# Optimization experiments

Measured on AMD Instinct MI355X. Metric: run time of the kernel, lower is better.

Reference implementation:

```python
import jax, jax.numpy as jnp
import numpy as np

N = 8192      # nodes
IN = 1433     # input_feat_dim
H1 = 256      # hidden_dim1
H2 = 128      # hidden_dim2
EPS = 1e-5    # BatchNorm1d eps
NEG = -9e15   # GAT mask value
SLOPE = 0.2   # leaky_relu negative slope (gamma)


def setup_inputs() -> dict:
    key = jax.random.key(0)
    ks = jax.random.split(key, 8)
    x = jax.random.normal(ks[0], (N, H2), dtype=jnp.float32)
    u = jax.random.uniform(ks[1], (N, N), dtype=jnp.float32)
    adj = jnp.where(u > 0.999, jnp.float32(0.01), jnp.float32(0.0))
    def w(k, shape):
        fan = shape[0]
        return jax.random.normal(k, shape, dtype=jnp.float32) / jnp.sqrt(jnp.float32(fan))
    return {
        "x": x,
        "adj": adj,
        "W_att": w(ks[2], (H2, H2)),
        "a_att": w(ks[3], (2 * H2, 1)),
        "W_fd1": w(ks[4], (H2, H1)),
        "bn1_g": jnp.ones((H1,), jnp.float32),
        "bn1_b": jnp.zeros((H1,), jnp.float32),
        "W_fd2": w(ks[5], (H1, IN)),
        "bn2_g": jnp.ones((IN,), jnp.float32),
        "bn2_b": jnp.zeros((IN,), jnp.float32),
        "W_sd1": w(ks[6], (H2, H1)),
        "bn3_g": jnp.ones((H1,), jnp.float32),
        "bn3_b": jnp.zeros((H1,), jnp.float32),
    }


def batchnorm(h, g, b):
    # BatchNorm1d training-mode forward: batch stats, biased variance
    m = h.mean(axis=0)
    v = ((h - m) ** 2).mean(axis=0)
    return (h - m) * jax.lax.rsqrt(v + EPS) * g + b


def reference(x, adj, W_att, a_att, W_fd1, bn1_g, bn1_b, W_fd2, bn2_g, bn2_b,
              W_sd1, bn3_g, bn3_b):
    # --- GraphAttentionLayer (concat=False, dropout=0) ---
    Wh = x @ W_att                       # [N, H2]
    f1 = Wh @ a_att[:H2]                 # [N, 1]
    f2 = Wh @ a_att[H2:]                 # [N, 1]
    e = jax.nn.leaky_relu(f1 + f2.T, SLOPE)          # [N, N]
    att = jnp.where(adj > 0, e, jnp.float32(NEG))
    att = jax.nn.softmax(att, axis=1)
    z = att @ Wh                         # condensed encoder output [N, H2]
    # --- feature decoder branch ---
    h1 = jax.nn.relu(adj @ (z @ W_fd1))  # GCN: adj @ (X W), relu
    h1 = batchnorm(h1, bn1_g, bn1_b)
    feat = jax.nn.relu(adj @ (h1 @ W_fd2))
    feat = batchnorm(feat, bn2_g, bn2_b)
    # --- structure decoder branch ---
    s1 = jax.nn.relu(adj @ (z @ W_sd1))
    s1 = batchnorm(s1, bn3_g, bn3_b)
    struct = s1 @ s1.T                   # inner-product decode, identity act [N, N]
    return feat, struct
```

## Files before the change

kernel.cpp:

```cpp
#include <hip/hip_runtime.h>
#include <hip/hip_bf16.h>
#include <stdint.h>

#define NN 8192
#define MAXNZ 64
#define BN_EPS 1e-5f
#define SLOPE 0.2f
#define IND 1433
#define NPAD 1536

typedef float f32x4v __attribute__((ext_vector_type(4)));
typedef short bf16x8v __attribute__((ext_vector_type(8)));

__device__ __forceinline__ float wave_sum(float v) {
#pragma unroll
  for (int off = 32; off > 0; off >>= 1) v += __shfl_xor(v, off);
  return v;
}
__device__ __forceinline__ float wave_max(float v) {
#pragma unroll
  for (int off = 32; off > 0; off >>= 1) v = fmaxf(v, __shfl_xor(v, off));
  return v;
}

#define GLOAD_LDS16(g, l)                                                      \
  __builtin_amdgcn_global_load_lds(                                            \
      (const __attribute__((address_space(1))) unsigned int*)(g),              \
      (__attribute__((address_space(3))) unsigned int*)(l), 16, 0, 0)

__global__ __launch_bounds__(256) void gemm64_f32(const float* __restrict__ A,
                                                  const float* __restrict__ B,
                                                  float* __restrict__ C, int M,
                                                  int N, int K) {
  __shared__ float As[64][68];
  __shared__ float Bs[64][68];
  const int t = threadIdx.x;
  const int m0 = blockIdx.x * 64, n0 = blockIdx.y * 64;
  const int tx = t & 15, ty = t >> 4;
  float acc[4][4] = {};
  for (int kt = 0; kt < K; kt += 64) {
    if (kt) __syncthreads();
#pragma unroll
    for (int i = 0; i < 4; ++i) {
      int fid = t + 256 * i;
      int r = fid >> 4, kq = (fid & 15) * 4;
      float4 v = *(const float4*)&A[(size_t)(m0 + r) * K + kt + kq];
      *(float4*)&As[r][kq] = v;
    }
#pragma unroll
    for (int i = 0; i < 4; ++i) {
      int fid = t + 256 * i;
      int r = fid >> 4, cq = (fid & 15) * 4;
      float4 v = *(const float4*)&B[(size_t)(kt + r) * N + n0 + cq];
      *(float4*)&Bs[r][cq] = v;
    }
    __syncthreads();
#pragma unroll 4
    for (int k0 = 0; k0 < 64; k0 += 4) {
      float4 a[4], b[4];
#pragma unroll
      for (int i = 0; i < 4; ++i) a[i] = *(const float4*)&As[ty * 4 + i][k0];
#pragma unroll
      for (int j = 0; j < 4; ++j) b[j] = *(const float4*)&Bs[k0 + j][tx * 4];
#pragma unroll
      for (int kk = 0; kk < 4; ++kk) {
#pragma unroll
        for (int i = 0; i < 4; ++i) {
          float av = ((const float*)&a[i])[kk];
#pragma unroll
          for (int j = 0; j < 4; ++j)
            acc[i][j] += av * ((const float*)&b[kk])[j];
        }
      }
    }
  }
#pragma unroll
  for (int i = 0; i < 4; ++i) {
    float4 v = make_float4(acc[i][0], acc[i][1], acc[i][2], acc[i][3]);
    *(float4*)&C[(size_t)(m0 + ty * 4 + i) * N + n0 + tx * 4] = v;
  }
}

__global__ void colsum_k(const float* __restrict__ Wh, float* __restrict__ cs) {
  int t = threadIdx.x, b = blockIdx.x;
  int c = t & 127, rg = t >> 7;
  float s = 0.f;
  int r0 = b * 128;
  for (int r = rg; r < 128; r += 2) s += Wh[(size_t)(r0 + r) * 128 + c];
  atomicAdd(&cs[c], s);
}

__global__ void f1f2_k(const float* __restrict__ Wh, const float* __restrict__ a_att,
                       float* __restrict__ f1, float* __restrict__ f2) {
  int l = threadIdx.x & 63, w = threadIdx.x >> 6;
  int i = blockIdx.x * 4 + w;
  float w0 = Wh[(size_t)i * 128 + l], w1 = Wh[(size_t)i * 128 + 64 + l];
  float p1 = w0 * a_att[l] + w1 * a_att[64 + l];
  float p2 = w0 * a_att[128 + l] + w1 * a_att[192 + l];
  p1 = wave_sum(p1);
  p2 = wave_sum(p2);
  if (l == 0) { f1[i] = p1; f2[i] = p2; }
}

__global__ void extract_attn_k(const float* __restrict__ adj, const float* __restrict__ Wh,
                               const float* __restrict__ f1, const float* __restrict__ f2,
                               const float* __restrict__ cs, int* __restrict__ nnzA,
                               int* __restrict__ idxA, float* __restrict__ valA,
                               float* __restrict__ valsumA, float* __restrict__ z) {
  __shared__ int idxL[4][MAXNZ];
  __shared__ float valL[4][MAXNZ];
  int l = threadIdx.x & 63, w = threadIdx.x >> 6;
  int i = blockIdx.x * 4 + w;
  const float* row = adj + (size_t)i * NN;
  int base = 0;
  for (int it = 0; it < NN / 256; ++it) {
    float4 v4 = *(const float4*)&row[it * 256 + l * 4];
#pragma unroll
    for (int j = 0; j < 4; ++j) {
      float v = ((const float*)&v4)[j];
      bool p = v > 0.0f;
      unsigned long long m = __ballot(p);
      if (p) {
        int pos = base + (int)__popcll(m & ((1ull << l) - 1ull));
        if (pos < MAXNZ) {
          idxL[w][pos] = it * 256 + l * 4 + j;
          valL[w][pos] = v;
        }
      }
      base += (int)__popcll(m);
    }
  }
  int nnz = base < MAXNZ ? base : MAXNZ;
  if (l == 0) nnzA[i] = nnz;
  __syncthreads();

  int c = -1;
  float v = 0.f, att = 0.f;
  if (l < nnz) { c = idxL[w][l]; v = valL[w][l]; }
  idxA[(size_t)i * MAXNZ + l] = (l < nnz) ? c : 0;
  valA[(size_t)i * MAXNZ + l] = v;
  float vs = wave_sum(v);
  if (l == 0) valsumA[i] = vs;

  if (nnz == 0) {
    const float inv = 1.0f / 8192.0f;
    z[(size_t)i * 128 + l] = cs[l] * inv;
    z[(size_t)i * 128 + 64 + l] = cs[64 + l] * inv;
    return;
  }
  float e = -INFINITY;
  if (l < nnz) {
    float u = f1[i] + f2[c];
    e = u >= 0.f ? u : SLOPE * u;
  }
  float mx = wave_max(e);
  float p = (l < nnz) ? expf(e - mx) : 0.f;
  float s = wave_sum(p);
  att = p / s;
  float a0 = 0.f, a1 = 0.f;
  for (int j = 0; j < nnz; ++j) {
    float wt = __shfl(att, j);
    int r = __shfl(c, j);
    a0 += wt * Wh[(size_t)r * 128 + l];
    a1 += wt * Wh[(size_t)r * 128 + 64 + l];
  }
  z[(size_t)i * 128 + l] = a0;
  z[(size_t)i * 128 + 64 + l] = a1;
}

__global__ void gather_z_k(const float* __restrict__ X, const int* __restrict__ nnzA,
                           const int* __restrict__ idxA, const float* __restrict__ valA,
                           __hip_bfloat16* __restrict__ Y) {
  int l = threadIdx.x & 63, w = threadIdx.x >> 6;
  int i = blockIdx.x * 4 + w;
  int nnz = nnzA[i];
  float a0 = 0.f, a1 = 0.f;
  for (int j = 0; j < nnz; ++j) {
    int r = idxA[(size_t)i * MAXNZ + j];
    float v = valA[(size_t)i * MAXNZ + j];
    a0 += v * X[(size_t)r * 128 + l];
    a1 += v * X[(size_t)r * 128 + 64 + l];
  }
  Y[(size_t)i * 128 + l] = __float2bfloat16(a0);
  Y[(size_t)i * 128 + 64 + l] = __float2bfloat16(a1);
}

__global__ void gather_h_k(const float* __restrict__ t, const int* __restrict__ nnzA,
                           const int* __restrict__ idxA, const float* __restrict__ valA,
                           const float* __restrict__ valsumA, const float* __restrict__ sums,
                           const float* __restrict__ sumsq, const float* __restrict__ g,
                           const float* __restrict__ b, __hip_bfloat16* __restrict__ Y) {
  __shared__ int idxL[MAXNZ];
  __shared__ float valL[MAXNZ];
  int i = blockIdx.x, tt = threadIdx.x;
  int nnz = nnzA[i];
  if (tt < MAXNZ) {
    idxL[tt] = idxA[(size_t)i * MAXNZ + tt];
    valL[tt] = valA[(size_t)i * MAXNZ + tt];
  }
  __syncthreads();
  float acc = 0.f;
  for (int j = 0; j < nnz; ++j)
    acc += valL[j] * fmaxf(t[(size_t)idxL[j] * 512 + tt], 0.f);
  float m = sums[tt] * (1.f / 8192.f);
  float va = fmaxf(sumsq[tt] * (1.f / 8192.f) - m * m, 0.f);
  float sc = g[tt] * rsqrtf(va + BN_EPS);
  float sh = b[tt] - m * sc;
  Y[(size_t)i * 256 + tt] = __float2bfloat16(acc * sc + sh * valsumA[i]);
}

__global__ void s1_apply_k(const float* __restrict__ t, const float* __restrict__ sums,
                           const float* __restrict__ sumsq, const float* __restrict__ g,
                           const float* __restrict__ b, __hip_bfloat16* __restrict__ s1b) {
  int i = blockIdx.x, c = threadIdx.x;
  float m = sums[256 + c] * (1.f / 8192.f);
  float va = fmaxf(sumsq[256 + c] * (1.f / 8192.f) - m * m, 0.f);
  float sc = g[c] * rsqrtf(va + BN_EPS);
  float sh = b[c] - m * sc;
  float v = fmaxf(t[(size_t)i * 512 + 256 + c], 0.f) * sc + sh;
  s1b[(size_t)i * 256 + c] = __float2bfloat16(v);
}

__global__ void feat_apply_k(const __hip_bfloat16* __restrict__ fp, const float* __restrict__ sums,
                             const float* __restrict__ sumsq, const float* __restrict__ g,
                             const float* __restrict__ b, float* __restrict__ out) {
  int i = blockIdx.x;
  for (int c = threadIdx.x; c < IND; c += 256) {
    float m = sums[c] * (1.f / 8192.f);
    float va = fmaxf(sumsq[c] * (1.f / 8192.f) - m * m, 0.f);
    float sc = g[c] * rsqrtf(va + BN_EPS);
    float sh = b[c] - m * sc;
    out[(size_t)i * IND + c] = __bfloat162float(fp[(size_t)i * NPAD + c]) * sc + sh;
  }
}

__global__ void prep_k(const float* __restrict__ W_fd2, const float* __restrict__ W_fd1,
                       const float* __restrict__ W_sd1, __hip_bfloat16* __restrict__ Wt,
                       __hip_bfloat16* __restrict__ Wcatb) {
  int b = blockIdx.x, t = threadIdx.x;
  int o = b * 256 + t;
  int n = o >> 8, k = o & 255;
  Wt[o] = __float2bfloat16(n < IND ? W_fd2[(size_t)k * IND + n] : 0.f);
  if (b < 256) {
    int nn = o >> 7, kk = o & 127;
    float v = nn < 256 ? W_fd1[(size_t)kk * 256 + nn] : W_sd1[(size_t)kk * 256 + (nn - 256)];
    Wcatb[o] = __float2bfloat16(v);
  }
}

template <int KT, int MODE>
__global__ __launch_bounds__(256) void mfma_bt_k(const short* __restrict__ A,
                                                 const short* __restrict__ Bt,
                                                 void* __restrict__ Cv, int ldc,
                                                 int gridN, float* __restrict__ sums,
                                                 float* __restrict__ sumsq) {
  __shared__ short lds[2][16384];
  const int nwg = gridDim.x;
  const int cpx = nwg >> 3;
  const int bid = blockIdx.x;
  const int wg = (bid & 7) * cpx + (bid >> 3);
  const int m0 = (wg / gridN) * 128, n0 = (wg % gridN) * 128;
  const int t = threadIdx.x;
  const int l = t & 63, w = t >> 6;
  const int wm = w >> 1, wn = w & 1;
  const int KW = KT * 128;
  f32x4v acc[4][4];
#pragma unroll
  for (int i = 0; i < 4; ++i)
#pragma unroll
    for (int j = 0; j < 4; ++j)
#pragma unroll
      for (int q = 0; q < 4; ++q) acc[i][j][q] = 0.f;

  for (int kt = 0; kt < KT; ++kt) {
    if (kt) __syncthreads();
#pragma unroll
    for (int i = 0; i < 8; ++i) {
      int region = w * 8 + i;
      int lr = region * 4 + (l >> 4);
      int ch = (l & 15) ^ (lr & 7);
      const short* gA = A + ((size_t)(m0 + lr) * KW + kt * 128 + ch * 8);
      GLOAD_LDS16(gA, &lds[0][region * 512]);
      const short* gB = Bt + ((size_t)(n0 + lr) * KW + kt * 128 + ch * 8);
      GLOAD_LDS16(gB, &lds[1][region * 512]);
    }
    __syncthreads();
#pragma unroll
    for (int ks = 0; ks < 4; ++ks) {
      bf16x8v af[4], bf[4];
#pragma unroll
      for (int mi = 0; mi < 4; ++mi) {
        int lr = wm * 64 + mi * 16 + (l & 15);
        int ch = (ks * 4 + (l >> 4)) ^ (lr & 7);
        af[mi] = *(const bf16x8v*)&lds[0][lr * 128 + ch * 8];
      }
#pragma unroll
      for (int nj = 0; nj < 4; ++nj) {
        int lr = wn * 64 + nj * 16 + (l & 15);
        int ch = (ks * 4 + (l >> 4)) ^ (lr & 7);
        bf[nj] = *(const bf16x8v*)&lds[1][lr * 128 + ch * 8];
      }
#pragma unroll
      for (int mi = 0; mi < 4; ++mi)
#pragma unroll
        for (int nj = 0; nj < 4; ++nj)
          acc[mi][nj] = __builtin_amdgcn_mfma_f32_16x16x32_bf16(
              af[mi], bf[nj], acc[mi][nj], 0, 0, 0);
    }
  }
#pragma unroll
  for (int nj = 0; nj < 4; ++nj) {
    int col = n0 + wn * 64 + nj * 16 + (l & 15);
    float s = 0.f, ss = 0.f;
#pragma unroll
    for (int mi = 0; mi < 4; ++mi) {
#pragma unroll
      for (int q = 0; q < 4; ++q) {
        int row = m0 + wm * 64 + mi * 16 + (l >> 4) * 4 + q;
        float raw = acc[mi][nj][q];
        float v = fmaxf(raw, 0.f);
        if (MODE == 1) {
          ((__hip_bfloat16*)Cv)[(size_t)row * ldc + col] = __float2bfloat16(v);
        } else {
          ((float*)Cv)[(size_t)row * ldc + col] = raw;
        }
        s += v;
        ss += v * v;
      }
    }
    s += __shfl_xor(s, 16);
    s += __shfl_xor(s, 32);
    ss += __shfl_xor(ss, 16);
    ss += __shfl_xor(ss, 32);
    if ((l >> 4) == 0) {
      atomicAdd(&sums[col], s);
      atomicAdd(&sumsq[col], ss);
    }
  }
}

__global__ __launch_bounds__(256) void mfma_sym_k(const short* __restrict__ A,
                                                  float* __restrict__ C) {
  __shared__ union {
    short stag[2][16384];
    float tr[64 * 129];
  } sh;
  const int bid = blockIdx.x;
  const int wg = (bid & 7) * 260 + (bid >> 3);
  int bi = (int)((129.0f - sqrtf(16641.0f - 8.0f * (float)wg)) * 0.5f);
  while ((bi + 1) * 64 - ((bi + 1) * bi) / 2 <= wg) ++bi;
  while (bi * 64 - (bi * (bi - 1)) / 2 > wg) --bi;
  const int bj = bi + (wg - (bi * 64 - (bi * (bi - 1)) / 2));
  const int m0 = bi * 128, n0 = bj * 128;
  const int t = threadIdx.x;
  const int l = t & 63, w = t >> 6;
  const int wm = w >> 1, wn = w & 1;
  f32x4v acc[4][4];
#pragma unroll
  for (int i = 0; i < 4; ++i)
#pragma unroll
    for (int j = 0; j < 4; ++j)
#pragma unroll
      for (int q = 0; q < 4; ++q) acc[i][j][q] = 0.f;

  for (int kt = 0; kt < 2; ++kt) {
    if (kt) __syncthreads();
#pragma unroll
    for (int i = 0; i < 8; ++i) {
      int region = w * 8 + i;
      int lr = region * 4 + (l >> 4);
      int ch = (l & 15) ^ (lr & 7);
      const short* gA = A + ((size_t)(m0 + lr) * 256 + kt * 128 + ch * 8);
      GLOAD_LDS16(gA, &sh.stag[0][region * 512]);
      const short* gB = A + ((size_t)(n0 + lr) * 256 + kt * 128 + ch * 8);
      GLOAD_LDS16(gB, &sh.stag[1][region * 512]);
    }
    __syncthreads();
#pragma unroll
    for (int ks = 0; ks < 4; ++ks) {
      bf16x8v af[4], bf[4];
#pragma unroll
      for (int mi = 0; mi < 4; ++mi) {
        int lr = wm * 64 + mi * 16 + (l & 15);
        int ch = (ks * 4 + (l >> 4)) ^ (lr & 7);
        af[mi] = *(const bf16x8v*)&sh.stag[0][lr * 128 + ch * 8];
      }
#pragma unroll
      for (int nj = 0; nj < 4; ++nj) {
        int lr = wn * 64 + nj * 16 + (l & 15);
        int ch = (ks * 4 + (l >> 4)) ^ (lr & 7);
        bf[nj] = *(const bf16x8v*)&sh.stag[1][lr * 128 + ch * 8];
      }
#pragma unroll
      for (int mi = 0; mi < 4; ++mi)
#pragma unroll
        for (int nj = 0; nj < 4; ++nj)
          acc[mi][nj] = __builtin_amdgcn_mfma_f32_16x16x32_bf16(
              af[mi], bf[nj], acc[mi][nj], 0, 0, 0);
    }
  }
#pragma unroll
  for (int mi = 0; mi < 4; ++mi) {
#pragma unroll
    for (int nj = 0; nj < 4; ++nj) {
      int col = n0 + wn * 64 + nj * 16 + (l & 15);
#pragma unroll
      for (int q = 0; q < 4; ++q) {
        int row = m0 + wm * 64 + mi * 16 + (l >> 4) * 4 + q;
        C[(size_t)row * NN + col] = acc[mi][nj][q];
      }
    }
  }
  if (bi != bj) {
    for (int half = 0; half < 2; ++half) {
      __syncthreads();
      if (wn == half) {
#pragma unroll
        for (int nj = 0; nj < 4; ++nj) {
          int cc = nj * 16 + (l & 15);
#pragma unroll
          for (int mi = 0; mi < 4; ++mi) {
#pragma unroll
            for (int q = 0; q < 4; ++q) {
              int rr = wm * 64 + mi * 16 + (l >> 4) * 4 + q;
              sh.tr[cc * 129 + rr] = acc[mi][nj][q];
            }
          }
        }
      }
      __syncthreads();
      for (int it = t; it < 64 * 32; it += 256) {
        int cc = it >> 5, rr = (it & 31) * 4;
        float4 v;
        v.x = sh.tr[cc * 129 + rr];
        v.y = sh.tr[cc * 129 + rr + 1];
        v.z = sh.tr[cc * 129 + rr + 2];
        v.w = sh.tr[cc * 129 + rr + 3];
        *(float4*)&C[(size_t)(n0 + half * 64 + cc) * NN + m0 + rr] = v;
      }
    }
  }
}

extern "C" void kernel_launch(void* const* d_in, const int* in_sizes, int n_in,
                              void* d_out, int out_size, void* d_ws, size_t ws_size,
                              hipStream_t stream) {
  const float* x = (const float*)d_in[0];
  const float* adj = (const float*)d_in[1];
  const float* W_att = (const float*)d_in[2];
  const float* a_att = (const float*)d_in[3];
  const float* W_fd1 = (const float*)d_in[4];
  const float* bn1g = (const float*)d_in[5];
  const float* bn1b = (const float*)d_in[6];
  const float* W_fd2 = (const float*)d_in[7];
  const float* bn2g = (const float*)d_in[8];
  const float* bn2b = (const float*)d_in[9];
  const float* W_sd1 = (const float*)d_in[10];
  const float* bn3g = (const float*)d_in[11];
  const float* bn3b = (const float*)d_in[12];

  float* out = (float*)d_out;
  float* feat_out = out;
  float* struct_out = out + (size_t)NN * IND;

  float* ws = (float*)d_ws;
  size_t off = 0;
  auto alloc = [&](size_t nfloats) {
    float* p = ws + off;
    off += (nfloats + 255) & ~(size_t)255;
    return p;
  };
  float* Wh = alloc((size_t)NN * 128);
  float* z = alloc((size_t)NN * 128);
  float* tbuf = alloc((size_t)NN * 512);
  float* f1 = alloc(NN);
  float* f2 = alloc(NN);
  float* valsum = alloc(NN);
  float* zbase = alloc(256 + 512 + 512 + 1536 + 1536);
  float* cs = zbase;
  float* sumsA = zbase + 256;
  float* sumsqA = zbase + 768;
  float* sumsB = zbase + 1280;
  float* sumsqB = zbase + 2816;
  float* valA = alloc((size_t)NN * MAXNZ);
  int* idxA = (int*)alloc((size_t)NN * MAXNZ);
  int* nnzA = (int*)alloc(NN);
  __hip_bfloat16* gb = (__hip_bfloat16*)alloc((size_t)NN * 64);
  __hip_bfloat16* s1b = (__hip_bfloat16*)alloc((size_t)NN * 128);
  __hip_bfloat16* ghb = (__hip_bfloat16*)alloc((size_t)NN * 128);
  __hip_bfloat16* Wt = (__hip_bfloat16*)alloc((size_t)NPAD * 128);
  __hip_bfloat16* Wcatb = (__hip_bfloat16*)alloc(512 * 64);
  __hip_bfloat16* featb = (__hip_bfloat16*)alloc((size_t)NN * NPAD / 2);

  hipMemsetAsync(zbase, 0, (256 + 512 + 512 + 1536 + 1536) * sizeof(float), stream);

  prep_k<<<NPAD, 256, 0, stream>>>(W_fd2, W_fd1, W_sd1, Wt, Wcatb);

  gemm64_f32<<<dim3(NN / 64, 2), 256, 0, stream>>>(x, W_att, Wh, NN, 128, 128);
  colsum_k<<<64, 256, 0, stream>>>(Wh, cs);
  f1f2_k<<<NN / 4, 256, 0, stream>>>(Wh, a_att, f1, f2);
  extract_attn_k<<<NN / 4, 256, 0, stream>>>(adj, Wh, f1, f2, cs, nnzA, idxA, valA,
                                             valsum, z);
  gather_z_k<<<NN / 4, 256, 0, stream>>>(z, nnzA, idxA, valA, gb);

  mfma_bt_k<1, 2><<<64 * 4, 256, 0, stream>>>((const short*)gb, (const short*)Wcatb,
                                              tbuf, 512, 4, sumsA, sumsqA);
  s1_apply_k<<<NN, 256, 0, stream>>>(tbuf, sumsA, sumsqA, bn3g, bn3b, s1b);
  gather_h_k<<<NN, 256, 0, stream>>>(tbuf, nnzA, idxA, valA, valsum, sumsA, sumsqA,
                                     bn1g, bn1b, ghb);

  mfma_bt_k<2, 1><<<64 * 12, 256, 0, stream>>>((const short*)ghb, (const short*)Wt,
                                               featb, NPAD, 12, sumsB, sumsqB);
  feat_apply_k<<<NN, 256, 0, stream>>>(featb, sumsB, sumsqB, bn2g, bn2b, feat_out);

  mfma_sym_k<<<2080, 256, 0, stream>>>((const short*)s1b, struct_out);
}
```

Baseline: 276.5 us.

## Fuse colsum/f1f2, merge s1 apply into gather, bf16 intermediate, direct sym stores

```diff
diff --git a/kernel.cpp b/kernel.cpp
--- a/kernel.cpp
+++ b/kernel.cpp
@@ -81,25 +81,29 @@
   }
 }
 
-__global__ void colsum_k(const float* __restrict__ Wh, float* __restrict__ cs) {
-  int t = threadIdx.x, b = blockIdx.x;
-  int c = t & 127, rg = t >> 7;
-  float s = 0.f;
-  int r0 = b * 128;
-  for (int r = rg; r < 128; r += 2) s += Wh[(size_t)(r0 + r) * 128 + c];
-  atomicAdd(&cs[c], s);
-}
-
-__global__ void f1f2_k(const float* __restrict__ Wh, const float* __restrict__ a_att,
-                       float* __restrict__ f1, float* __restrict__ f2) {
-  int l = threadIdx.x & 63, w = threadIdx.x >> 6;
-  int i = blockIdx.x * 4 + w;
-  float w0 = Wh[(size_t)i * 128 + l], w1 = Wh[(size_t)i * 128 + 64 + l];
-  float p1 = w0 * a_att[l] + w1 * a_att[64 + l];
-  float p2 = w0 * a_att[128 + l] + w1 * a_att[192 + l];
-  p1 = wave_sum(p1);
-  p2 = wave_sum(p2);
-  if (l == 0) { f1[i] = p1; f2[i] = p2; }
+__global__ void colf_k(const float* __restrict__ Wh, const float* __restrict__ a_att,
+                       float* __restrict__ cs, float* __restrict__ f1,
+                       float* __restrict__ f2) {
+  __shared__ float csL[128];
+  int t = threadIdx.x, l = t & 63, w = t >> 6;
+  if (t < 128) csL[t] = 0.f;
+  __syncthreads();
+  float a0 = a_att[l], a1 = a_att[64 + l], a2 = a_att[128 + l], a3 = a_att[192 + l];
+  float s0 = 0.f, s1 = 0.f;
+#pragma unroll
+  for (int rr = 0; rr < 4; ++rr) {
+    int i = blockIdx.x * 16 + w * 4 + rr;
+    float w0 = Wh[(size_t)i * 128 + l], w1 = Wh[(size_t)i * 128 + 64 + l];
+    s0 += w0;
+    s1 += w1;
+    float p1 = wave_sum(w0 * a0 + w1 * a1);
+    float p2 = wave_sum(w0 * a2 + w1 * a3);
+    if (l == 0) { f1[i] = p1; f2[i] = p2; }
+  }
+  atomicAdd(&csL[l], s0);
+  atomicAdd(&csL[64 + l], s1);
+  __syncthreads();
+  if (t < 128) atomicAdd(&cs[t], csL[t]);
 }
 
 __global__ void extract_attn_k(const float* __restrict__ adj, const float* __restrict__ Wh,
@@ -185,11 +189,13 @@
   Y[(size_t)i * 128 + 64 + l] = __float2bfloat16(a1);
 }
 
-__global__ void gather_h_k(const float* __restrict__ t, const int* __restrict__ nnzA,
-                           const int* __restrict__ idxA, const float* __restrict__ valA,
-                           const float* __restrict__ valsumA, const float* __restrict__ sums,
-                           const float* __restrict__ sumsq, const float* __restrict__ g,
-                           const float* __restrict__ b, __hip_bfloat16* __restrict__ Y) {
+__global__ void s1_gather_k(const __hip_bfloat16* __restrict__ t, const int* __restrict__ nnzA,
+                            const int* __restrict__ idxA, const float* __restrict__ valA,
+                            const float* __restrict__ valsumA, const float* __restrict__ sums,
+                            const float* __restrict__ sumsq, const float* __restrict__ g1,
+                            const float* __restrict__ b1, const float* __restrict__ g3,
+                            const float* __restrict__ b3, __hip_bfloat16* __restrict__ s1b,
+                            __hip_bfloat16* __restrict__ ghb) {
   __shared__ int idxL[MAXNZ];
   __shared__ float valL[MAXNZ];
   int i = blockIdx.x, tt = threadIdx.x;
@@ -199,26 +205,22 @@
     valL[tt] = valA[(size_t)i * MAXNZ + tt];
   }
   __syncthreads();
+  {
+    float m = sums[256 + tt] * (1.f / 8192.f);
+    float va = fmaxf(sumsq[256 + tt] * (1.f / 8192.f) - m * m, 0.f);
+    float sc = g3[tt] * rsqrtf(va + BN_EPS);
+    float sh = b3[tt] - m * sc;
+    float v = __bfloat162float(t[(size_t)i * 512 + 256 + tt]) * sc + sh;
+    s1b[(size_t)i * 256 + tt] = __float2bfloat16(v);
+  }
   float acc = 0.f;
   for (int j = 0; j < nnz; ++j)
-    acc += valL[j] * fmaxf(t[(size_t)idxL[j] * 512 + tt], 0.f);
+    acc += valL[j] * __bfloat162float(t[(size_t)idxL[j] * 512 + tt]);
   float m = sums[tt] * (1.f / 8192.f);
   float va = fmaxf(sumsq[tt] * (1.f / 8192.f) - m * m, 0.f);
-  float sc = g[tt] * rsqrtf(va + BN_EPS);
-  float sh = b[tt] - m * sc;
-  Y[(size_t)i * 256 + tt] = __float2bfloat16(acc * sc + sh * valsumA[i]);
-}
-
-__global__ void s1_apply_k(const float* __restrict__ t, const float* __restrict__ sums,
-                           const float* __restrict__ sumsq, const float* __restrict__ g,
-                           const float* __restrict__ b, __hip_bfloat16* __restrict__ s1b) {
-  int i = blockIdx.x, c = threadIdx.x;
-  float m = sums[256 + c] * (1.f / 8192.f);
-  float va = fmaxf(sumsq[256 + c] * (1.f / 8192.f) - m * m, 0.f);
-  float sc = g[c] * rsqrtf(va + BN_EPS);
-  float sh = b[c] - m * sc;
-  float v = fmaxf(t[(size_t)i * 512 + 256 + c], 0.f) * sc + sh;
-  s1b[(size_t)i * 256 + c] = __float2bfloat16(v);
+  float sc = g1[tt] * rsqrtf(va + BN_EPS);
+  float sh = b1[tt] - m * sc;
+  ghb[(size_t)i * 256 + tt] = __float2bfloat16(acc * sc + sh * valsumA[i]);
 }
 
 __global__ void feat_apply_k(const __hip_bfloat16* __restrict__ fp, const float* __restrict__ sums,
@@ -248,10 +250,10 @@
   }
 }
 
-template <int KT, int MODE>
+template <int KT>
 __global__ __launch_bounds__(256) void mfma_bt_k(const short* __restrict__ A,
                                                  const short* __restrict__ Bt,
-                                                 void* __restrict__ Cv, int ldc,
+                                                 __hip_bfloat16* __restrict__ C, int ldc,
                                                  int gridN, float* __restrict__ sums,
                                                  float* __restrict__ sumsq) {
   __shared__ short lds[2][16384];
@@ -317,13 +319,8 @@
 #pragma unroll
       for (int q = 0; q < 4; ++q) {
         int row = m0 + wm * 64 + mi * 16 + (l >> 4) * 4 + q;
-        float raw = acc[mi][nj][q];
-        float v = fmaxf(raw, 0.f);
-        if (MODE == 1) {
-          ((__hip_bfloat16*)Cv)[(size_t)row * ldc + col] = __float2bfloat16(v);
-        } else {
-          ((float*)Cv)[(size_t)row * ldc + col] = raw;
-        }
+        float v = fmaxf(acc[mi][nj][q], 0.f);
+        C[(size_t)row * ldc + col] = __float2bfloat16(v);
         s += v;
         ss += v * v;
       }
@@ -341,10 +338,7 @@
 
 __global__ __launch_bounds__(256) void mfma_sym_k(const short* __restrict__ A,
                                                   float* __restrict__ C) {
-  __shared__ union {
-    short stag[2][16384];
-    float tr[64 * 129];
-  } sh;
+  __shared__ short stag[2][16384];
   const int bid = blockIdx.x;
   const int wg = (bid & 7) * 260 + (bid >> 3);
   int bi = (int)((129.0f - sqrtf(16641.0f - 8.0f * (float)wg)) * 0.5f);
@@ -371,9 +365,9 @@
       int lr = region * 4 + (l >> 4);
       int ch = (l & 15) ^ (lr & 7);
       const short* gA = A + ((size_t)(m0 + lr) * 256 + kt * 128 + ch * 8);
-      GLOAD_LDS16(gA, &sh.stag[0][region * 512]);
+      GLOAD_LDS16(gA, &stag[0][region * 512]);
       const short* gB = A + ((size_t)(n0 + lr) * 256 + kt * 128 + ch * 8);
-      GLOAD_LDS16(gB, &sh.stag[1][region * 512]);
+      GLOAD_LDS16(gB, &stag[1][region * 512]);
     }
     __syncthreads();
 #pragma unroll
@@ -383,13 +377,13 @@
       for (int mi = 0; mi < 4; ++mi) {
         int lr = wm * 64 + mi * 16 + (l & 15);
         int ch = (ks * 4 + (l >> 4)) ^ (lr & 7);
-        af[mi] = *(const bf16x8v*)&sh.stag[0][lr * 128 + ch * 8];
+        af[mi] = *(const bf16x8v*)&stag[0][lr * 128 + ch * 8];
       }
 #pragma unroll
       for (int nj = 0; nj < 4; ++nj) {
         int lr = wn * 64 + nj * 16 + (l & 15);
         int ch = (ks * 4 + (l >> 4)) ^ (lr & 7);
-        bf[nj] = *(const bf16x8v*)&sh.stag[1][lr * 128 + ch * 8];
+        bf[nj] = *(const bf16x8v*)&stag[1][lr * 128 + ch * 8];
       }
 #pragma unroll
       for (int mi = 0; mi < 4; ++mi)
@@ -412,31 +406,15 @@
     }
   }
   if (bi != bj) {
-    for (int half = 0; half < 2; ++half) {
-      __syncthreads();
-      if (wn == half) {
-#pragma unroll
-        for (int nj = 0; nj < 4; ++nj) {
-          int cc = nj * 16 + (l & 15);
-#pragma unroll
-          for (int mi = 0; mi < 4; ++mi) {
-#pragma unroll
-            for (int q = 0; q < 4; ++q) {
-              int rr = wm * 64 + mi * 16 + (l >> 4) * 4 + q;
-              sh.tr[cc * 129 + rr] = acc[mi][nj][q];
-            }
-          }
-        }
-      }
-      __syncthreads();
-      for (int it = t; it < 64 * 32; it += 256) {
-        int cc = it >> 5, rr = (it & 31) * 4;
-        float4 v;
-        v.x = sh.tr[cc * 129 + rr];
-        v.y = sh.tr[cc * 129 + rr + 1];
-        v.z = sh.tr[cc * 129 + rr + 2];
-        v.w = sh.tr[cc * 129 + rr + 3];
-        *(float4*)&C[(size_t)(n0 + half * 64 + cc) * NN + m0 + rr] = v;
+#pragma unroll
+    for (int nj = 0; nj < 4; ++nj) {
+      int col = n0 + wn * 64 + nj * 16 + (l & 15);
+#pragma unroll
+      for (int mi = 0; mi < 4; ++mi) {
+        int row0 = m0 + wm * 64 + mi * 16 + (l >> 4) * 4;
+        float4 v = make_float4(acc[mi][nj][0], acc[mi][nj][1], acc[mi][nj][2],
+                               acc[mi][nj][3]);
+        *(float4*)&C[(size_t)col * NN + row0] = v;
       }
     }
   }
@@ -472,7 +450,6 @@
   };
   float* Wh = alloc((size_t)NN * 128);
   float* z = alloc((size_t)NN * 128);
-  float* tbuf = alloc((size_t)NN * 512);
   float* f1 = alloc(NN);
   float* f2 = alloc(NN);
   float* valsum = alloc(NN);
@@ -485,6 +462,7 @@
   float* valA = alloc((size_t)NN * MAXNZ);
   int* idxA = (int*)alloc((size_t)NN * MAXNZ);
   int* nnzA = (int*)alloc(NN);
+  __hip_bfloat16* tbuf = (__hip_bfloat16*)alloc((size_t)NN * 256);
   __hip_bfloat16* gb = (__hip_bfloat16*)alloc((size_t)NN * 64);
   __hip_bfloat16* s1b = (__hip_bfloat16*)alloc((size_t)NN * 128);
   __hip_bfloat16* ghb = (__hip_bfloat16*)alloc((size_t)NN * 128);
@@ -497,20 +475,18 @@
   prep_k<<<NPAD, 256, 0, stream>>>(W_fd2, W_fd1, W_sd1, Wt, Wcatb);
 
   gemm64_f32<<<dim3(NN / 64, 2), 256, 0, stream>>>(x, W_att, Wh, NN, 128, 128);
-  colsum_k<<<64, 256, 0, stream>>>(Wh, cs);
-  f1f2_k<<<NN / 4, 256, 0, stream>>>(Wh, a_att, f1, f2);
+  colf_k<<<NN / 16, 256, 0, stream>>>(Wh, a_att, cs, f1, f2);
   extract_attn_k<<<NN / 4, 256, 0, stream>>>(adj, Wh, f1, f2, cs, nnzA, idxA, valA,
                                              valsum, z);
   gather_z_k<<<NN / 4, 256, 0, stream>>>(z, nnzA, idxA, valA, gb);
 
-  mfma_bt_k<1, 2><<<64 * 4, 256, 0, stream>>>((const short*)gb, (const short*)Wcatb,
-                                              tbuf, 512, 4, sumsA, sumsqA);
-  s1_apply_k<<<NN, 256, 0, stream>>>(tbuf, sumsA, sumsqA, bn3g, bn3b, s1b);
-  gather_h_k<<<NN, 256, 0, stream>>>(tbuf, nnzA, idxA, valA, valsum, sumsA, sumsqA,
-                                     bn1g, bn1b, ghb);
-
-  mfma_bt_k<2, 1><<<64 * 12, 256, 0, stream>>>((const short*)ghb, (const short*)Wt,
-                                               featb, NPAD, 12, sumsB, sumsqB);
+  mfma_bt_k<1><<<64 * 4, 256, 0, stream>>>((const short*)gb, (const short*)Wcatb,
+                                           tbuf, 512, 4, sumsA, sumsqA);
+  s1_gather_k<<<NN, 256, 0, stream>>>(tbuf, nnzA, idxA, valA, valsum, sumsA, sumsqA,
+                                      bn1g, bn1b, bn3g, bn3b, s1b, ghb);
+
+  mfma_bt_k<2><<<64 * 12, 256, 0, stream>>>((const short*)ghb, (const short*)Wt,
+                                            featb, NPAD, 12, sumsB, sumsqB);
   feat_apply_k<<<NN, 256, 0, stream>>>(featb, sumsB, sumsqB, bn2g, bn2b, feat_out);
 
   mfma_sym_k<<<2080, 256, 0, stream>>>((const short*)s1b, struct_out);
```

After: 255.7 us. 7.5% less time.
